# Kernel optimization log

Hardware: AMD Instinct MI355X
Metric: run time of the kernel (lower is better)

The kernel has to match this reference:

```python
import jax, jax.numpy as jnp
import numpy as np
from jax import lax

N_NODES = 100000
L_IN = 60           # raw per-node signal length
DEG = 16            # in-degree per node
HID = 256           # hidden_dim = 64 * (L_IN/15)
HEADS = 2
OUT = HID // 2      # GATConv out_feats per head
EPS_BN = 1e-5
COS_S = 4.6


def setup_inputs() -> dict:
    key = jax.random.key(0)
    k = jax.random.split(key, 12)
    E = N_NODES * DEG
    x = jax.random.normal(k[0], (N_NODES, L_IN), jnp.float32)
    src = jax.random.randint(k[1], (E,), 0, N_NODES, jnp.int32)
    # every node receives DEG incoming edges (DGL GATConv requires nonzero in-degree)
    dst = jnp.repeat(jnp.arange(N_NODES, dtype=jnp.int32), DEG)
    n = lambda i, s, sc=0.05: jax.random.normal(k[i], s, jnp.float32) * sc
    return dict(
        x=x, src=src, dst=dst,
        w1=n(2, (32, 1, 5), 0.2), b1=jnp.zeros(32, jnp.float32),
        bn1_g=jnp.ones(32, jnp.float32), bn1_b=jnp.zeros(32, jnp.float32),
        w2=n(3, (64, 32, 3), 0.1), b2=jnp.zeros(64, jnp.float32),
        bn2_g=jnp.ones(64, jnp.float32), bn2_b=jnp.zeros(64, jnp.float32),
        fc1_w=n(4, (HEADS * OUT, HID)), attn1_l=n(5, (HEADS, OUT)), attn1_r=n(6, (HEADS, OUT)),
        bias1=jnp.zeros(HEADS * OUT, jnp.float32),
        fc2_w=n(7, (HEADS * OUT, HID)), attn2_l=n(8, (HEADS, OUT)), attn2_r=n(9, (HEADS, OUT)),
        bias2=jnp.zeros(HEADS * OUT, jnp.float32),
        dbn_g=jnp.ones(3 * HID, jnp.float32), dbn_b=jnp.zeros(3 * HID, jnp.float32),
        cos_W=n(10, (HID, 3 * HID), 1.0),
    )


def _conv_bn_relu(h, w, b, g, bt, stride):
    # h: [N, Cin, T] -> [N, Cout, T'] ; BatchNorm1d uses batch statistics (train-mode forward)
    y = lax.conv_general_dilated(h, w, (stride,), 'VALID',
                                 dimension_numbers=('NCH', 'OIH', 'NCH'))
    y = y + b[None, :, None]
    m = jnp.mean(y, (0, 2), keepdims=True)
    v = jnp.var(y, (0, 2), keepdims=True)
    y = (y - m) / jnp.sqrt(v + EPS_BN) * g[None, :, None] + bt[None, :, None]
    return jax.nn.relu(y)


def _gat(h, fc_w, al, ar, bias, src, dst):
    # DGL GATConv: fc -> edge attention (leaky_relu 0.2) -> edge softmax over dst -> weighted sum + bias
    feat = (h @ fc_w.T).reshape(N_NODES, HEADS, OUT)          # [N,H,D]
    el = jnp.sum(feat * al[None], -1)                          # [N,H]
    er = jnp.sum(feat * ar[None], -1)                          # [N,H]
    e = jax.nn.leaky_relu(el[src] + er[dst], 0.2)              # [E,H]
    emax = jax.ops.segment_max(e, dst, num_segments=N_NODES)  # [N,H]
    emax = jnp.where(jnp.isfinite(emax), emax, 0.0)
    ex = jnp.exp(e - emax[dst])
    den = jax.ops.segment_sum(ex, dst, num_segments=N_NODES)  # [N,H]
    alpha = ex / jnp.maximum(den[dst], 1e-12)                  # [E,H]
    out = jax.ops.segment_sum(feat[src] * alpha[..., None], dst, num_segments=N_NODES)
    return out + bias.reshape(1, HEADS, OUT)                   # [N,H,D]


def _l2n(a):
    # F.normalize: divide by L2 norm clamped to eps
    return a / jnp.maximum(jnp.linalg.norm(a, axis=1, keepdims=True), 1e-12)


def reference(x, src, dst, w1, b1, bn1_g, bn1_b, w2, b2, bn2_g, bn2_b,
              fc1_w, attn1_l, attn1_r, bias1, fc2_w, attn2_l, attn2_r, bias2,
              dbn_g, dbn_b, cos_W):
    h = x[:, None, :]                                    # [N,1,L]
    h = _conv_bn_relu(h, w1, b1, bn1_g, bn1_b, 5)        # [N,32,12]
    h = _conv_bn_relu(h, w2, b2, bn2_g, bn2_b, 3)        # [N,64,4]
    h = h.reshape(N_NODES, HID)                          # [N,256]
    g1 = _gat(h, fc1_w, attn1_l, attn1_r, bias1, src, dst)
    h1 = (jax.nn.relu(g1) + jnp.tanh(g1) + jax.nn.log_sigmoid(g1)).reshape(N_NODES, HID)
    h2 = jnp.tanh(_gat(h1, fc2_w, attn2_l, attn2_r, bias2, src, dst)).reshape(N_NODES, HID)
    h3 = jax.nn.relu(_gat(h2, fc2_w, attn2_l, attn2_r, bias2, src, dst)).reshape(N_NODES, HID)
    hc = jnp.concatenate([h1, h2, h3], axis=1)           # [N,768]
    m = jnp.mean(hc, 0)
    v = jnp.var(hc, 0)
    hc = (hc - m) / jnp.sqrt(v + EPS_BN) * dbn_g + dbn_b
    return _l2n(hc) @ _l2n(cos_W).T * COS_S              # [N,256]
```

## Files before the change

### kernel.cpp

```cpp
#include <hip/hip_runtime.h>

#define NN 100000
#define MPAD 100096
#define NT_M 782

typedef unsigned short u16;
typedef __attribute__((ext_vector_type(8))) short bf16x8;
typedef __attribute__((ext_vector_type(4))) float f32x4;

__device__ __forceinline__ u16 f2bf(float f){
  union { float f; unsigned u; } v; v.f=f;
  unsigned u = v.u + 0x7fffu + ((v.u>>16)&1u);
  return (u16)(u>>16);
}
__device__ __forceinline__ float bf2f(u16 b){
  union { unsigned u; float f; } v; v.u = ((unsigned)b)<<16; return v.f;
}
__device__ __forceinline__ void gload16(const void* g, void* l){
  __builtin_amdgcn_global_load_lds((const __attribute__((address_space(1))) void*)g,
                                   (__attribute__((address_space(3))) void*)l, 16, 0, 0);
}
__device__ __forceinline__ void lds_fence(){
  asm volatile("s_waitcnt lgkmcnt(0)" ::: "memory");
  __builtin_amdgcn_wave_barrier();
}

template<int EPI>
__global__ __launch_bounds__(256) void k_gemm(
  const u16* __restrict__ ah0, const u16* __restrict__ al0,
  const u16* __restrict__ ah1, const u16* __restrict__ al1,
  const u16* __restrict__ ah2, const u16* __restrict__ al2,
  const u16* __restrict__ bh, const u16* __restrict__ bl,
  u16* __restrict__ chi,
  float* __restrict__ outf, const float* __restrict__ tvec,
  const float* __restrict__ rnorm, int Bstride, int KT)
{
  __shared__ u16 lds[2][4][4096];
  const int tid=threadIdx.x, lane=tid&63, wid=tid>>6;
  const int wr=wid>>1, wc=wid&1;
  const long m0=(long)blockIdx.x*128;
  const int n0=blockIdx.y*128;
  f32x4 acc[4][4]={};

  auto stageT=[&](u16* L, const u16* G, int rs){
    #pragma unroll
    for(int i=0;i<2;i++){
      int idx=i*256+tid;
      int row=idx>>2, c8=idx&3;
      int gc=(c8^(row&3))*8;
      gload16(G+(long)row*rs+gc, L+idx*8);
    }
  };
  auto stage=[&](int buf,int kt){
    const u16 *Ah,*Al; int kc;
    if(kt<8){Ah=ah0;Al=al0;kc=kt*32;}
    else if(kt<16){Ah=ah1;Al=al1;kc=(kt-8)*32;}
    else {Ah=ah2;Al=al2;kc=(kt-16)*32;}
    stageT(lds[buf][0], Ah+m0*256+kc, 256);
    stageT(lds[buf][1], Al+m0*256+kc, 256);
    stageT(lds[buf][2], bh+(long)n0*Bstride+kt*32, Bstride);
    stageT(lds[buf][3], bl+(long)n0*Bstride+kt*32, Bstride);
  };
  stage(0,0);
  __syncthreads();
  int buf=0;
  for(int kt=0;kt<KT;kt++){
    if(kt+1<KT) stage(buf^1,kt+1);
    const u16* LAh=lds[buf][0]; const u16* LAl=lds[buf][1];
    const u16* LBh=lds[buf][2]; const u16* LBl=lds[buf][3];
    bf16x8 avh[4],avl[4],bvh[4],bvl[4];
    #pragma unroll
    for(int mf=0;mf<4;mf++){
      int r=wr*64+mf*16+(lane&15);
      int ch=((lane>>4)^(r&3))*8;
      avh[mf]=*(const bf16x8*)&LAh[r*32+ch];
      avl[mf]=*(const bf16x8*)&LAl[r*32+ch];
    }
    #pragma unroll
    for(int nf=0;nf<4;nf++){
      int r=wc*64+nf*16+(lane&15);
      int ch=((lane>>4)^(r&3))*8;
      bvh[nf]=*(const bf16x8*)&LBh[r*32+ch];
      bvl[nf]=*(const bf16x8*)&LBl[r*32+ch];
    }
    #pragma unroll
    for(int mf=0;mf<4;mf++){
      #pragma unroll
      for(int nf=0;nf<4;nf++){
        acc[mf][nf]=__builtin_amdgcn_mfma_f32_16x16x32_bf16(avh[mf],bvh[nf],acc[mf][nf],0,0,0);
        acc[mf][nf]=__builtin_amdgcn_mfma_f32_16x16x32_bf16(avl[mf],bvh[nf],acc[mf][nf],0,0,0);
        acc[mf][nf]=__builtin_amdgcn_mfma_f32_16x16x32_bf16(avh[mf],bvl[nf],acc[mf][nf],0,0,0);
      }
    }
    __syncthreads();
    buf^=1;
  }
  #pragma unroll
  for(int mf=0;mf<4;mf++){
    #pragma unroll
    for(int j=0;j<4;j++){
      long row=m0+wr*64+mf*16+((lane>>4)*4)+j;
      if(row<NN){
        #pragma unroll
        for(int nf=0;nf<4;nf++){
          int col=n0+wc*64+nf*16+(lane&15);
          float v=acc[mf][nf][j];
          if(EPI==1) outf[row*256+col]=(v+tvec[col])*rnorm[row];
          else       chi[row*256+col]=f2bf(v);
        }
      }
    }
  }
}

__global__ __launch_bounds__(256) void k_xmom(const float* __restrict__ x, float* __restrict__ stats){
  int t=blockIdx.x*blockDim.x+threadIdx.x, stride=gridDim.x*blockDim.x;
  int lane=threadIdx.x&63;
  float m[5]={0,0,0,0,0};
  float c[15]={0,0,0,0,0,0,0,0,0,0,0,0,0,0,0};
  for(int n=t;n<NN;n+=stride){
    float xr[60];
    #pragma unroll
    for(int i=0;i<15;i++){
      float4 v=*(const float4*)&x[(long)n*60+i*4];
      xr[i*4]=v.x; xr[i*4+1]=v.y; xr[i*4+2]=v.z; xr[i*4+3]=v.w;
    }
    #pragma unroll
    for(int p=0;p<12;p++){
      float vv[5]={xr[5*p],xr[5*p+1],xr[5*p+2],xr[5*p+3],xr[5*p+4]};
      #pragma unroll
      for(int k=0;k<5;k++) m[k]+=vv[k];
      int idx=0;
      #pragma unroll
      for(int k=0;k<5;k++){
        #pragma unroll
        for(int k2=k;k2<5;k2++){ c[idx]+=vv[k]*vv[k2]; idx++; }
      }
    }
  }
  float vals[20];
  #pragma unroll
  for(int i=0;i<5;i++) vals[i]=m[i];
  #pragma unroll
  for(int i=0;i<15;i++) vals[5+i]=c[i];
  #pragma unroll
  for(int i=0;i<20;i++){
    float v=vals[i];
    #pragma unroll
    for(int off=32;off;off>>=1) v+=__shfl_xor(v,off);
    if(lane==0) atomicAdd(&stats[i],v);
  }
}

__global__ void k_fin1(const float* __restrict__ stats, const float* __restrict__ w1,
                       const float* __restrict__ b1, const float* __restrict__ g,
                       const float* __restrict__ bt, float* __restrict__ a1c1){
  int c=threadIdx.x;
  if(c>=32) return;
  const float inv=1.0f/(NN*12.0f);
  float mu[5];
  for(int k=0;k<5;k++) mu[k]=stats[k]*inv;
  float C[5][5];
  int idx=5;
  for(int k=0;k<5;k++) for(int k2=k;k2<5;k2++){ float v=stats[idx++]*inv; C[k][k2]=v; C[k2][k]=v; }
  float wv[5];
  for(int k=0;k<5;k++) wv[k]=w1[c*5+k];
  float bb=b1[c];
  float mean=bb, e2=bb*bb;
  for(int k=0;k<5;k++){ mean+=wv[k]*mu[k]; e2+=2.f*bb*wv[k]*mu[k]; }
  for(int k=0;k<5;k++) for(int k2=0;k2<5;k2++) e2+=wv[k]*wv[k2]*C[k][k2];
  float var=e2-mean*mean;
  float a=g[c]*rsqrtf(var+1e-5f);
  a1c1[c]=a; a1c1[32+c]=bt[c]-mean*a;
}

__global__ void k_prep(const float* __restrict__ fc1, const float* __restrict__ fc2,
                       const float* __restrict__ a1l, const float* __restrict__ a1r,
                       const float* __restrict__ a2l, const float* __restrict__ a2r,
                       float* __restrict__ vprep){
  int k=threadIdx.x;
  float acc[8]={0,0,0,0,0,0,0,0};
  for(int r=0;r<256;r++){
    int h=r>>7, c=r&127;
    float f1=fc1[r*256+k], f2=fc2[r*256+k];
    acc[0+h]+=f1*a1l[h*128+c];
    acc[2+h]+=f1*a1r[h*128+c];
    acc[4+h]+=f2*a2l[h*128+c];
    acc[6+h]+=f2*a2r[h*128+c];
  }
  #pragma unroll
  for(int v=0;v<8;v++) vprep[v*256+k]=acc[v];
}

template<int PASS>
__global__ __launch_bounds__(256) void k_conv(const float* __restrict__ x,
  const float* __restrict__ w1, const float* __restrict__ b1,
  const float* __restrict__ a1c1, const float* __restrict__ w2,
  const float* __restrict__ b2, const float* __restrict__ a2c2,
  u16* __restrict__ hH, u16* __restrict__ hL, float* __restrict__ stats2,
  const float* __restrict__ vprep, float* __restrict__ elv, float* __restrict__ erv)
{
  __shared__ float w2s[64*97];
  __shared__ float w1s[160], a1s[32], c1s[32], b1s[32], b2s[64];
  __shared__ float xs[4][64];
  __shared__ float z1s[4][384];
  __shared__ float bsum[128];
  int tid=threadIdx.x, lane=tid&63, w=tid>>6;
  for(int i=tid;i<6144;i+=256) w2s[(i/96)*97+(i%96)]=w2[i];
  if(tid<160) w1s[tid]=w1[tid];
  if(tid<32){ a1s[tid]=a1c1[tid]; c1s[tid]=a1c1[32+tid]; b1s[tid]=b1[tid]; }
  if(tid<64) b2s[tid]=b2[tid];
  if(PASS==0 && tid<128) bsum[tid]=0.f;
  __syncthreads();
  float ssum=0.f, ssq=0.f;
  float a2=0.f, c2v=0.f;
  float4 vl0={0,0,0,0},vl1={0,0,0,0},vr0={0,0,0,0},vr1={0,0,0,0};
  if(PASS==1){
    a2=a2c2[lane]; c2v=a2c2[64+lane];
    int cb=lane*4;
    vl0=*(const float4*)&vprep[cb];
    vl1=*(const float4*)&vprep[256+cb];
    vr0=*(const float4*)&vprep[512+cb];
    vr1=*(const float4*)&vprep[768+cb];
  }
  int gw=blockIdx.x*4+w, nw=gridDim.x*4;
  for(int n=gw;n<NN;n+=nw){
    if(lane<60) xs[w][lane]=x[(long)n*60+lane];
    lds_fence();
    {
      int c=lane>>1, pb=(lane&1)*6;
      float av=a1s[c], cv=c1s[c], bb=b1s[c];
      #pragma unroll
      for(int i=0;i<6;i++){
        int p=pb+i;
        float y=bb;
        #pragma unroll
        for(int k=0;k<5;k++) y+=xs[w][5*p+k]*w1s[c*5+k];
        z1s[w][c*12+p]=fmaxf(y*av+cv,0.f);
      }
    }
    lds_fence();
    {
      int c2=lane;
      float acc0=b2s[c2],acc1=b2s[c2],acc2=b2s[c2],acc3=b2s[c2];
      #pragma unroll
      for(int ci=0;ci<32;ci++){
        float4 za=*(const float4*)&z1s[w][ci*12];
        float4 zb=*(const float4*)&z1s[w][ci*12+4];
        float4 zc=*(const float4*)&z1s[w][ci*12+8];
        float w0=w2s[c2*97+ci*3], wv1=w2s[c2*97+ci*3+1], wv2=w2s[c2*97+ci*3+2];
        acc0 += za.x*w0+za.y*wv1+za.z*wv2;
        acc1 += za.w*w0+zb.x*wv1+zb.y*wv2;
        acc2 += zb.z*w0+zb.w*wv1+zc.x*wv2;
        acc3 += zc.y*w0+zc.z*wv1+zc.w*wv2;
      }
      if(PASS==0){
        ssum+=acc0+acc1+acc2+acc3;
        ssq+=acc0*acc0+acc1*acc1+acc2*acc2+acc3*acc3;
      } else {
        float o0=fmaxf(acc0*a2+c2v,0.f), o1=fmaxf(acc1*a2+c2v,0.f);
        float o2=fmaxf(acc2*a2+c2v,0.f), o3=fmaxf(acc3*a2+c2v,0.f);
        ushort4 hi, lo;
        hi.x=f2bf(o0); lo.x=f2bf(o0-bf2f(hi.x));
        hi.y=f2bf(o1); lo.y=f2bf(o1-bf2f(hi.y));
        hi.z=f2bf(o2); lo.z=f2bf(o2-bf2f(hi.z));
        hi.w=f2bf(o3); lo.w=f2bf(o3-bf2f(hi.w));
        *(ushort4*)&hH[(long)n*256+c2*4]=hi;
        *(ushort4*)&hL[(long)n*256+c2*4]=lo;
        float pl0=o0*vl0.x+o1*vl0.y+o2*vl0.z+o3*vl0.w;
        float pl1=o0*vl1.x+o1*vl1.y+o2*vl1.z+o3*vl1.w;
        float pr0=o0*vr0.x+o1*vr0.y+o2*vr0.z+o3*vr0.w;
        float pr1=o0*vr1.x+o1*vr1.y+o2*vr1.z+o3*vr1.w;
        #pragma unroll
        for(int off2=32;off2;off2>>=1){
          pl0+=__shfl_xor(pl0,off2); pl1+=__shfl_xor(pl1,off2);
          pr0+=__shfl_xor(pr0,off2); pr1+=__shfl_xor(pr1,off2);
        }
        if(lane==0){ elv[2*n]=pl0; elv[2*n+1]=pl1; erv[2*n]=pr0; erv[2*n+1]=pr1; }
      }
    }
    lds_fence();
  }
  if(PASS==0){
    atomicAdd(&bsum[lane],ssum);
    atomicAdd(&bsum[64+lane],ssq);
    __syncthreads();
    if(tid<128) atomicAdd(&stats2[tid],bsum[tid]);
  }
}

__global__ void k_fin2(const float* __restrict__ stats2, const float* __restrict__ g,
                       const float* __restrict__ bt, float* __restrict__ a2c2){
  int c=threadIdx.x;
  if(c>=64) return;
  const float inv=1.0f/(NN*4.0f);
  float mean=stats2[c]*inv;
  float var=stats2[64+c]*inv-mean*mean;
  float a=g[c]*rsqrtf(var+1e-5f);
  a2c2[c]=a; a2c2[64+c]=bt[c]-mean*a;
}

__global__ void k_cvt2(const float* __restrict__ in, u16* __restrict__ oh, u16* __restrict__ ol, int n){
  int i=blockIdx.x*blockDim.x+threadIdx.x;
  if(i<n){
    float v=in[i];
    u16 h=f2bf(v);
    oh[i]=h; ol[i]=f2bf(v-bf2f(h));
  }
}

__global__ __launch_bounds__(256) void k_wfold(const float* __restrict__ cw, const float* __restrict__ ab,
  u16* __restrict__ wh, u16* __restrict__ wl, float* __restrict__ tvec)
{
  int lane=threadIdx.x&63;
  int r=blockIdx.x*4+(threadIdx.x>>6);
  if(r>=256) return;
  float v[12]; float ss=0.f, tn=0.f;
  #pragma unroll
  for(int i=0;i<12;i++){
    int col=i*64+lane;
    v[i]=cw[r*768+col];
    ss+=v[i]*v[i];
    tn+=v[i]*ab[768+col];
  }
  #pragma unroll
  for(int off=32;off;off>>=1){ ss+=__shfl_xor(ss,off); tn+=__shfl_xor(tn,off); }
  float sc=1.0f/fmaxf(sqrtf(ss),1e-12f);
  #pragma unroll
  for(int i=0;i<12;i++){
    int col=i*64+lane;
    float wv=v[i]*sc*ab[col];
    u16 h=f2bf(wv);
    wh[r*768+col]=h; wl[r*768+col]=f2bf(wv-bf2f(h));
  }
  if(lane==0) tvec[r]=tn*sc;
}

__global__ __launch_bounds__(256) void k_alpha(const float* __restrict__ el, const float* __restrict__ er,
  const int* __restrict__ srcv, float* __restrict__ alpha)
{
  int n=blockIdx.x*blockDim.x+threadIdx.x;
  if(n>=NN) return;
  int sidx[16];
  #pragma unroll
  for(int j=0;j<16;j+=4){
    int4 v=*(const int4*)&srcv[n*16+j];
    sidx[j]=v.x; sidx[j+1]=v.y; sidx[j+2]=v.z; sidx[j+3]=v.w;
  }
  float er0=er[2*n], er1=er[2*n+1];
  float e0[16], e1[16];
  float mx0=-1e30f, mx1=-1e30f;
  #pragma unroll
  for(int j=0;j<16;j++){
    float a=el[2*sidx[j]]+er0;
    float bb=el[2*sidx[j]+1]+er1;
    a = a>0.f? a : 0.2f*a;
    bb = bb>0.f? bb : 0.2f*bb;
    e0[j]=a; e1[j]=bb;
    mx0=fmaxf(mx0,a); mx1=fmaxf(mx1,bb);
  }
  float d0=0.f,d1=0.f;
  #pragma unroll
  for(int j=0;j<16;j++){
    e0[j]=__expf(e0[j]-mx0); d0+=e0[j];
    e1[j]=__expf(e1[j]-mx1); d1+=e1[j];
  }
  float r0=1.f/fmaxf(d0,1e-12f), r1=1.f/fmaxf(d1,1e-12f);
  #pragma unroll
  for(int j=0;j<16;j++){
    float2 o; o.x=e0[j]*r0; o.y=e1[j]*r1;
    ((float2*)alpha)[(long)n*16+j]=o;
  }
}

template<int ACT> __device__ __forceinline__ float actf(float g);
template<> __device__ __forceinline__ float actf<1>(float g){
  float t=tanhf(g);
  float ls=fminf(g,0.f)-log1pf(__expf(-fabsf(g)));
  return fmaxf(g,0.f)+t+ls;
}
template<> __device__ __forceinline__ float actf<2>(float g){ return tanhf(g); }
template<> __device__ __forceinline__ float actf<3>(float g){ return fmaxf(g,0.f); }

template<int ACT,int WELR>
__global__ __launch_bounds__(256) void k_aggr(const u16* __restrict__ fH,
  const float* __restrict__ alpha, const int* __restrict__ srcv, const float* __restrict__ bias,
  u16* __restrict__ hH, u16* __restrict__ hL, float* __restrict__ dbn_raw, int col_base,
  const float* __restrict__ vnext, float* __restrict__ elo, float* __restrict__ ero)
{
  __shared__ float bsum[256], bsq[256];
  int tid=threadIdx.x, lane=tid&63;
  bsum[tid]=0.f; bsq[tid]=0.f;
  __syncthreads();
  int gw=blockIdx.x*4+(tid>>6), nw=gridDim.x*4;
  int head=lane>>5, cb=lane*4;
  float4 b4=*(const float4*)&bias[cb];
  float4 vl0={0,0,0,0},vl1={0,0,0,0},vr0={0,0,0,0},vr1={0,0,0,0};
  if(WELR){
    vl0=*(const float4*)&vnext[cb];
    vl1=*(const float4*)&vnext[256+cb];
    vr0=*(const float4*)&vnext[512+cb];
    vr1=*(const float4*)&vnext[768+cb];
  }
  float s[4]={0,0,0,0}, q[4]={0,0,0,0};
  for(int n=gw;n<NN;n+=nw){
    int sidx[16];
    #pragma unroll
    for(int j=0;j<16;j+=4){
      int4 v=*(const int4*)&srcv[n*16+j];
      sidx[j]=v.x; sidx[j+1]=v.y; sidx[j+2]=v.z; sidx[j+3]=v.w;
    }
    float a0=b4.x,a1=b4.y,a2=b4.z,a3=b4.w;
    #pragma unroll
    for(int j=0;j<16;j++){
      float2 aw2=((const float2*)alpha)[(long)n*16+j];
      float aw = head? aw2.y : aw2.x;
      ushort4 f=*(const ushort4*)&fH[(long)sidx[j]*256+cb];
      a0+=aw*bf2f(f.x); a1+=aw*bf2f(f.y);
      a2+=aw*bf2f(f.z); a3+=aw*bf2f(f.w);
    }
    float h0=actf<ACT>(a0), h1=actf<ACT>(a1), h2=actf<ACT>(a2), h3=actf<ACT>(a3);
    ushort4 hi, lo;
    hi.x=f2bf(h0); lo.x=f2bf(h0-bf2f(hi.x));
    hi.y=f2bf(h1); lo.y=f2bf(h1-bf2f(hi.y));
    hi.z=f2bf(h2); lo.z=f2bf(h2-bf2f(hi.z));
    hi.w=f2bf(h3); lo.w=f2bf(h3-bf2f(hi.w));
    *(ushort4*)&hH[(long)n*256+cb]=hi;
    *(ushort4*)&hL[(long)n*256+cb]=lo;
    s[0]+=h0; s[1]+=h1; s[2]+=h2; s[3]+=h3;
    q[0]+=h0*h0; q[1]+=h1*h1; q[2]+=h2*h2; q[3]+=h3*h3;
    if(WELR){
      float pl0=h0*vl0.x+h1*vl0.y+h2*vl0.z+h3*vl0.w;
      float pl1=h0*vl1.x+h1*vl1.y+h2*vl1.z+h3*vl1.w;
      float pr0=h0*vr0.x+h1*vr0.y+h2*vr0.z+h3*vr0.w;
      float pr1=h0*vr1.x+h1*vr1.y+h2*vr1.z+h3*vr1.w;
      #pragma unroll
      for(int off2=32;off2;off2>>=1){
        pl0+=__shfl_xor(pl0,off2); pl1+=__shfl_xor(pl1,off2);
        pr0+=__shfl_xor(pr0,off2); pr1+=__shfl_xor(pr1,off2);
      }
      if(lane==0){ elo[2*n]=pl0; elo[2*n+1]=pl1; ero[2*n]=pr0; ero[2*n+1]=pr1; }
    }
  }
  #pragma unroll
  for(int i=0;i<4;i++){ atomicAdd(&bsum[cb+i], s[i]); atomicAdd(&bsq[cb+i], q[i]); }
  __syncthreads();
  atomicAdd(&dbn_raw[col_base+tid], bsum[tid]);
  atomicAdd(&dbn_raw[768+col_base+tid], bsq[tid]);
}

__global__ void k_dbnfin(const float* __restrict__ raw, const float* __restrict__ g,
                         const float* __restrict__ b, float* __restrict__ ab){
  int c=blockIdx.x*blockDim.x+threadIdx.x;
  if(c<768){
    float mean=raw[c]*(1.0f/NN);
    float var=raw[768+c]*(1.0f/NN)-mean*mean;
    float a=g[c]*rsqrtf(var+1e-5f);
    ab[c]=a; ab[768+c]=b[c]-mean*a;
  }
}

__global__ __launch_bounds__(256) void k_rnorm(
  const u16* __restrict__ h1h, const u16* __restrict__ h1l,
  const u16* __restrict__ h2h, const u16* __restrict__ h2l,
  const u16* __restrict__ h3h, const u16* __restrict__ h3l,
  const float* __restrict__ ab, float* __restrict__ rn)
{
  int lane=threadIdx.x&63;
  int gw=blockIdx.x*4+(threadIdx.x>>6), nw=gridDim.x*4;
  int cb=lane*4;
  float av[12], cv[12];
  #pragma unroll
  for(int s=0;s<3;s++){
    #pragma unroll
    for(int i=0;i<4;i++){ av[s*4+i]=ab[s*256+cb+i]; cv[s*4+i]=ab[768+s*256+cb+i]; }
  }
  for(int n=gw;n<NN;n+=nw){
    float ss=0.f;
    const u16* hh[3]={h1h,h2h,h3h};
    const u16* hl[3]={h1l,h2l,h3l};
    #pragma unroll
    for(int s=0;s<3;s++){
      ushort4 a4=*(const ushort4*)&hh[s][(long)n*256+cb];
      ushort4 c4=*(const ushort4*)&hl[s][(long)n*256+cb];
      float o0=(bf2f(a4.x)+bf2f(c4.x))*av[s*4+0]+cv[s*4+0];
      float o1=(bf2f(a4.y)+bf2f(c4.y))*av[s*4+1]+cv[s*4+1];
      float o2=(bf2f(a4.z)+bf2f(c4.z))*av[s*4+2]+cv[s*4+2];
      float o3=(bf2f(a4.w)+bf2f(c4.w))*av[s*4+3]+cv[s*4+3];
      ss+=o0*o0+o1*o1+o2*o2+o3*o3;
    }
    #pragma unroll
    for(int off=32;off;off>>=1) ss+=__shfl_xor(ss,off);
    if(lane==0) rn[n]=4.6f/fmaxf(sqrtf(ss),1e-12f);
  }
}

extern "C" void kernel_launch(void* const* d_in, const int* in_sizes, int n_in,
                              void* d_out, int out_size, void* d_ws, size_t ws_size,
                              hipStream_t stream)
{
  (void)in_sizes; (void)n_in; (void)out_size; (void)ws_size;
  const float* x   =(const float*)d_in[0];
  const int*   src =(const int*)d_in[1];
  const float* w1  =(const float*)d_in[3];
  const float* b1  =(const float*)d_in[4];
  const float* bn1g=(const float*)d_in[5];
  const float* bn1b=(const float*)d_in[6];
  const float* w2  =(const float*)d_in[7];
  const float* b2  =(const float*)d_in[8];
  const float* bn2g=(const float*)d_in[9];
  const float* bn2b=(const float*)d_in[10];
  const float* fc1 =(const float*)d_in[11];
  const float* a1l =(const float*)d_in[12];
  const float* a1r =(const float*)d_in[13];
  const float* bias1=(const float*)d_in[14];
  const float* fc2 =(const float*)d_in[15];
  const float* a2l =(const float*)d_in[16];
  const float* a2r =(const float*)d_in[17];
  const float* bias2=(const float*)d_in[18];
  const float* dbng=(const float*)d_in[19];
  const float* dbnb=(const float*)d_in[20];
  const float* cw  =(const float*)d_in[21];

  char* ws=(char*)d_ws;
  size_t off=0;
  auto take=[&](size_t bytes)->char*{ char* p=ws+off; off=(off+bytes+255)&~(size_t)255; return p; };
  float* stats =(float*)take(2048*4);
  float* params=(float*)take(4096*4);
  float* el    =(float*)take((size_t)MPAD*2*4);
  float* er    =(float*)take((size_t)MPAD*2*4);
  float* rnorm =(float*)take((size_t)MPAD*4);
  float* tvec  =(float*)take(256*4);
  float* alpha =(float*)take((size_t)NN*32*4);
  u16* fc1h=(u16*)take((size_t)65536*2);
  u16* fc1l=(u16*)take((size_t)65536*2);
  u16* fc2h=(u16*)take((size_t)65536*2);
  u16* fc2l=(u16*)take((size_t)65536*2);
  u16* wfh =(u16*)take((size_t)196608*2);
  u16* wfl =(u16*)take((size_t)196608*2);
  const size_t FB=(size_t)MPAD*256*2;
  u16* h0H  =(u16*)take(FB); u16* h0L  =(u16*)take(FB);
  u16* h1H  =(u16*)take(FB); u16* h1L  =(u16*)take(FB);
  u16* h2H  =(u16*)take(FB); u16* h2L  =(u16*)take(FB);
  u16* featH=(u16*)d_out;

  float* xmom   =stats;
  float* stats2 =stats+32;
  float* dbn_raw=stats+512;
  float* a1c1   =params;
  float* a2c2   =params+64;
  float* dbn_ab =params+256;
  float* vprep  =params+2048;

  hipMemsetAsync(stats,0,2048*4,stream);
  k_cvt2<<<dim3(256),dim3(256),0,stream>>>(fc1,fc1h,fc1l,65536);
  k_cvt2<<<dim3(256),dim3(256),0,stream>>>(fc2,fc2h,fc2l,65536);
  k_prep<<<dim3(1),dim3(256),0,stream>>>(fc1,fc2,a1l,a1r,a2l,a2r,vprep);
  k_xmom<<<dim3(128),dim3(256),0,stream>>>(x,xmom);
  k_fin1<<<dim3(1),dim3(64),0,stream>>>(xmom,w1,b1,bn1g,bn1b,a1c1);
  k_conv<0><<<dim3(1024),dim3(256),0,stream>>>(x,w1,b1,a1c1,w2,b2,a2c2,h0H,h0L,stats2,vprep,el,er);
  k_fin2<<<dim3(1),dim3(64),0,stream>>>(stats2,bn2g,bn2b,a2c2);
  k_conv<1><<<dim3(1024),dim3(256),0,stream>>>(x,w1,b1,a1c1,w2,b2,a2c2,h0H,h0L,stats2,vprep,el,er);

  dim3 gg(NT_M,2);
  k_gemm<0><<<gg,dim3(256),0,stream>>>(h0H,h0L,h0H,h0L,h0H,h0L,fc1h,fc1l,featH,
                                       (float*)nullptr,tvec,rnorm,256,8);
  k_alpha<<<dim3(391),dim3(256),0,stream>>>(el,er,src,alpha);
  k_aggr<1,1><<<dim3(2048),dim3(256),0,stream>>>(featH,alpha,src,bias1,h1H,h1L,dbn_raw,0,
                                                 vprep+1024,el,er);
  k_gemm<0><<<gg,dim3(256),0,stream>>>(h1H,h1L,h1H,h1L,h1H,h1L,fc2h,fc2l,featH,
                                       (float*)nullptr,tvec,rnorm,256,8);
  k_alpha<<<dim3(391),dim3(256),0,stream>>>(el,er,src,alpha);
  k_aggr<2,1><<<dim3(2048),dim3(256),0,stream>>>(featH,alpha,src,bias2,h2H,h2L,dbn_raw,256,
                                                 vprep+1024,el,er);
  k_gemm<0><<<gg,dim3(256),0,stream>>>(h2H,h2L,h2H,h2L,h2H,h2L,fc2h,fc2l,featH,
                                       (float*)nullptr,tvec,rnorm,256,8);
  k_alpha<<<dim3(391),dim3(256),0,stream>>>(el,er,src,alpha);
  k_aggr<3,0><<<dim3(2048),dim3(256),0,stream>>>(featH,alpha,src,bias2,h0H,h0L,dbn_raw,512,
                                                 vprep+1024,el,er);
  k_dbnfin<<<dim3(3),dim3(256),0,stream>>>(dbn_raw,dbng,dbnb,dbn_ab);
  k_wfold<<<dim3(64),dim3(256),0,stream>>>(cw,dbn_ab,wfh,wfl,tvec);
  k_rnorm<<<dim3(1024),dim3(256),0,stream>>>(h1H,h1L,h2H,h2L,h0H,h0L,dbn_ab,rnorm);
  k_gemm<1><<<gg,dim3(256),0,stream>>>(h1H,h1L,h2H,h2L,h0H,h0L,wfh,wfl,(u16*)nullptr,
                                       (float*)d_out,tvec,rnorm,768,24);
}
```

Baseline: 1.572 ms.

## Replace split-bf16 hi/lo GEMMs with single fp16 operands and split conv pass

Replaces the three-MFMA split-bf16 (hi/lo) emulation of fp32 GEMMs with a single fp16 MFMA per fragment, widens the K tile to 64 with an 8-way swizzle, and drops all low-part activation and weight buffers. The second conv pass, which recomputed conv1/conv2, now stores fp32 conv2 outputs once and a new elementwise kernel applies BN/ReLU and computes el/er. This removes about two thirds of the MFMA work and halves activation traffic for the GEMM operands and the aggregation, rnorm and final steps. In exchange, precision drops to single fp16 (about 11 bits of mantissa, with limited range) and a 100MB fp32 intermediate is written and read.

```diff
diff --git a/kernel.cpp b/kernel.cpp
--- a/kernel.cpp
+++ b/kernel.cpp
@@ -5,16 +5,14 @@
 #define NT_M 782
 
 typedef unsigned short u16;
-typedef __attribute__((ext_vector_type(8))) short bf16x8;
+typedef _Float16 f16x8 __attribute__((ext_vector_type(8)));
 typedef __attribute__((ext_vector_type(4))) float f32x4;
 
-__device__ __forceinline__ u16 f2bf(float f){
-  union { float f; unsigned u; } v; v.f=f;
-  unsigned u = v.u + 0x7fffu + ((v.u>>16)&1u);
-  return (u16)(u>>16);
-}
-__device__ __forceinline__ float bf2f(u16 b){
-  union { unsigned u; float f; } v; v.u = ((unsigned)b)<<16; return v.f;
+__device__ __forceinline__ u16 f2h(float f){
+  union { _Float16 h; u16 u; } v; v.h=(_Float16)f; return v.u;
+}
+__device__ __forceinline__ float h2f(u16 u){
+  union { u16 u; _Float16 h; } v; v.u=u; return (float)v.h;
 }
 __device__ __forceinline__ void gload16(const void* g, void* l){
   __builtin_amdgcn_global_load_lds((const __attribute__((address_space(1))) void*)g,
@@ -27,69 +25,57 @@
 
 template<int EPI>
 __global__ __launch_bounds__(256) void k_gemm(
-  const u16* __restrict__ ah0, const u16* __restrict__ al0,
-  const u16* __restrict__ ah1, const u16* __restrict__ al1,
-  const u16* __restrict__ ah2, const u16* __restrict__ al2,
-  const u16* __restrict__ bh, const u16* __restrict__ bl,
-  u16* __restrict__ chi,
+  const u16* __restrict__ a0, const u16* __restrict__ a1, const u16* __restrict__ a2,
+  const u16* __restrict__ bmat, u16* __restrict__ cout,
   float* __restrict__ outf, const float* __restrict__ tvec,
   const float* __restrict__ rnorm, int Bstride, int KT)
 {
-  __shared__ u16 lds[2][4][4096];
+  __shared__ u16 lds[2][2][8192];
   const int tid=threadIdx.x, lane=tid&63, wid=tid>>6;
   const int wr=wid>>1, wc=wid&1;
   const long m0=(long)blockIdx.x*128;
   const int n0=blockIdx.y*128;
   f32x4 acc[4][4]={};
 
-  auto stageT=[&](u16* L, const u16* G, int rs){
-    #pragma unroll
-    for(int i=0;i<2;i++){
+  auto stageT=[&](u16* L, const u16* G, long rs){
+    #pragma unroll
+    for(int i=0;i<4;i++){
       int idx=i*256+tid;
-      int row=idx>>2, c8=idx&3;
-      int gc=(c8^(row&3))*8;
+      int row=idx>>3, slot=idx&7;
+      int gc=(slot^(row&7))*8;
       gload16(G+(long)row*rs+gc, L+idx*8);
     }
   };
   auto stage=[&](int buf,int kt){
-    const u16 *Ah,*Al; int kc;
-    if(kt<8){Ah=ah0;Al=al0;kc=kt*32;}
-    else if(kt<16){Ah=ah1;Al=al1;kc=(kt-8)*32;}
-    else {Ah=ah2;Al=al2;kc=(kt-16)*32;}
-    stageT(lds[buf][0], Ah+m0*256+kc, 256);
-    stageT(lds[buf][1], Al+m0*256+kc, 256);
-    stageT(lds[buf][2], bh+(long)n0*Bstride+kt*32, Bstride);
-    stageT(lds[buf][3], bl+(long)n0*Bstride+kt*32, Bstride);
+    const u16* Ab=(kt<4)?a0:((kt<8)?a1:a2);
+    int kc=(kt&3)*64;
+    stageT(lds[buf][0], Ab+m0*256+kc, 256);
+    stageT(lds[buf][1], bmat+(long)n0*Bstride+kt*64, Bstride);
   };
   stage(0,0);
   __syncthreads();
   int buf=0;
   for(int kt=0;kt<KT;kt++){
     if(kt+1<KT) stage(buf^1,kt+1);
-    const u16* LAh=lds[buf][0]; const u16* LAl=lds[buf][1];
-    const u16* LBh=lds[buf][2]; const u16* LBl=lds[buf][3];
-    bf16x8 avh[4],avl[4],bvh[4],bvl[4];
-    #pragma unroll
-    for(int mf=0;mf<4;mf++){
-      int r=wr*64+mf*16+(lane&15);
-      int ch=((lane>>4)^(r&3))*8;
-      avh[mf]=*(const bf16x8*)&LAh[r*32+ch];
-      avl[mf]=*(const bf16x8*)&LAl[r*32+ch];
-    }
-    #pragma unroll
-    for(int nf=0;nf<4;nf++){
-      int r=wc*64+nf*16+(lane&15);
-      int ch=((lane>>4)^(r&3))*8;
-      bvh[nf]=*(const bf16x8*)&LBh[r*32+ch];
-      bvl[nf]=*(const bf16x8*)&LBl[r*32+ch];
-    }
-    #pragma unroll
-    for(int mf=0;mf<4;mf++){
+    const u16* LA=lds[buf][0]; const u16* LB=lds[buf][1];
+    #pragma unroll
+    for(int kk=0;kk<2;kk++){
+      f16x8 av[4], bv[4];
+      #pragma unroll
+      for(int mf=0;mf<4;mf++){
+        int r=wr*64+mf*16+(lane&15);
+        av[mf]=*(const f16x8*)&LA[r*64 + (((kk*4+(lane>>4))^(r&7))*8)];
+      }
       #pragma unroll
       for(int nf=0;nf<4;nf++){
-        acc[mf][nf]=__builtin_amdgcn_mfma_f32_16x16x32_bf16(avh[mf],bvh[nf],acc[mf][nf],0,0,0);
-        acc[mf][nf]=__builtin_amdgcn_mfma_f32_16x16x32_bf16(avl[mf],bvh[nf],acc[mf][nf],0,0,0);
-        acc[mf][nf]=__builtin_amdgcn_mfma_f32_16x16x32_bf16(avh[mf],bvl[nf],acc[mf][nf],0,0,0);
+        int r=wc*64+nf*16+(lane&15);
+        bv[nf]=*(const f16x8*)&LB[r*64 + (((kk*4+(lane>>4))^(r&7))*8)];
+      }
+      #pragma unroll
+      for(int mf=0;mf<4;mf++){
+        #pragma unroll
+        for(int nf=0;nf<4;nf++)
+          acc[mf][nf]=__builtin_amdgcn_mfma_f32_16x16x32_f16(av[mf],bv[nf],acc[mf][nf],0,0,0);
       }
     }
     __syncthreads();
@@ -106,7 +92,7 @@
           int col=n0+wc*64+nf*16+(lane&15);
           float v=acc[mf][nf][j];
           if(EPI==1) outf[row*256+col]=(v+tvec[col])*rnorm[row];
-          else       chi[row*256+col]=f2bf(v);
+          else       cout[row*256+col]=f2h(v);
         }
       }
     }
@@ -192,13 +178,10 @@
   for(int v=0;v<8;v++) vprep[v*256+k]=acc[v];
 }
 
-template<int PASS>
 __global__ __launch_bounds__(256) void k_conv(const float* __restrict__ x,
   const float* __restrict__ w1, const float* __restrict__ b1,
   const float* __restrict__ a1c1, const float* __restrict__ w2,
-  const float* __restrict__ b2, const float* __restrict__ a2c2,
-  u16* __restrict__ hH, u16* __restrict__ hL, float* __restrict__ stats2,
-  const float* __restrict__ vprep, float* __restrict__ elv, float* __restrict__ erv)
+  const float* __restrict__ b2, float* __restrict__ y2, float* __restrict__ stats2)
 {
   __shared__ float w2s[64*97];
   __shared__ float w1s[160], a1s[32], c1s[32], b1s[32], b2s[64];
@@ -210,19 +193,9 @@
   if(tid<160) w1s[tid]=w1[tid];
   if(tid<32){ a1s[tid]=a1c1[tid]; c1s[tid]=a1c1[32+tid]; b1s[tid]=b1[tid]; }
   if(tid<64) b2s[tid]=b2[tid];
-  if(PASS==0 && tid<128) bsum[tid]=0.f;
+  if(tid<128) bsum[tid]=0.f;
   __syncthreads();
   float ssum=0.f, ssq=0.f;
-  float a2=0.f, c2v=0.f;
-  float4 vl0={0,0,0,0},vl1={0,0,0,0},vr0={0,0,0,0},vr1={0,0,0,0};
-  if(PASS==1){
-    a2=a2c2[lane]; c2v=a2c2[64+lane];
-    int cb=lane*4;
-    vl0=*(const float4*)&vprep[cb];
-    vl1=*(const float4*)&vprep[256+cb];
-    vr0=*(const float4*)&vprep[512+cb];
-    vr1=*(const float4*)&vprep[768+cb];
-  }
   int gw=blockIdx.x*4+w, nw=gridDim.x*4;
   for(int n=gw;n<NN;n+=nw){
     if(lane<60) xs[w][lane]=x[(long)n*60+lane];
@@ -254,39 +227,17 @@
         acc2 += zb.z*w0+zb.w*wv1+zc.x*wv2;
         acc3 += zc.y*w0+zc.z*wv1+zc.w*wv2;
       }
-      if(PASS==0){
-        ssum+=acc0+acc1+acc2+acc3;
-        ssq+=acc0*acc0+acc1*acc1+acc2*acc2+acc3*acc3;
-      } else {
-        float o0=fmaxf(acc0*a2+c2v,0.f), o1=fmaxf(acc1*a2+c2v,0.f);
-        float o2=fmaxf(acc2*a2+c2v,0.f), o3=fmaxf(acc3*a2+c2v,0.f);
-        ushort4 hi, lo;
-        hi.x=f2bf(o0); lo.x=f2bf(o0-bf2f(hi.x));
-        hi.y=f2bf(o1); lo.y=f2bf(o1-bf2f(hi.y));
-        hi.z=f2bf(o2); lo.z=f2bf(o2-bf2f(hi.z));
-        hi.w=f2bf(o3); lo.w=f2bf(o3-bf2f(hi.w));
-        *(ushort4*)&hH[(long)n*256+c2*4]=hi;
-        *(ushort4*)&hL[(long)n*256+c2*4]=lo;
-        float pl0=o0*vl0.x+o1*vl0.y+o2*vl0.z+o3*vl0.w;
-        float pl1=o0*vl1.x+o1*vl1.y+o2*vl1.z+o3*vl1.w;
-        float pr0=o0*vr0.x+o1*vr0.y+o2*vr0.z+o3*vr0.w;
-        float pr1=o0*vr1.x+o1*vr1.y+o2*vr1.z+o3*vr1.w;
-        #pragma unroll
-        for(int off2=32;off2;off2>>=1){
-          pl0+=__shfl_xor(pl0,off2); pl1+=__shfl_xor(pl1,off2);
-          pr0+=__shfl_xor(pr0,off2); pr1+=__shfl_xor(pr1,off2);
-        }
-        if(lane==0){ elv[2*n]=pl0; elv[2*n+1]=pl1; erv[2*n]=pr0; erv[2*n+1]=pr1; }
-      }
+      float4 o; o.x=acc0; o.y=acc1; o.z=acc2; o.w=acc3;
+      *(float4*)&y2[(long)n*256+c2*4]=o;
+      ssum+=acc0+acc1+acc2+acc3;
+      ssq+=acc0*acc0+acc1*acc1+acc2*acc2+acc3*acc3;
     }
     lds_fence();
   }
-  if(PASS==0){
-    atomicAdd(&bsum[lane],ssum);
-    atomicAdd(&bsum[64+lane],ssq);
-    __syncthreads();
-    if(tid<128) atomicAdd(&stats2[tid],bsum[tid]);
-  }
+  atomicAdd(&bsum[lane],ssum);
+  atomicAdd(&bsum[64+lane],ssq);
+  __syncthreads();
+  if(tid<128) atomicAdd(&stats2[tid],bsum[tid]);
 }
 
 __global__ void k_fin2(const float* __restrict__ stats2, const float* __restrict__ g,
@@ -300,17 +251,44 @@
   a2c2[c]=a; a2c2[64+c]=bt[c]-mean*a;
 }
 
-__global__ void k_cvt2(const float* __restrict__ in, u16* __restrict__ oh, u16* __restrict__ ol, int n){
+__global__ __launch_bounds__(256) void k_happ(const float* __restrict__ y2,
+  const float* __restrict__ a2c2, const float* __restrict__ vprep,
+  u16* __restrict__ h, float* __restrict__ elv, float* __restrict__ erv)
+{
+  int lane=threadIdx.x&63;
+  int gw=blockIdx.x*4+(threadIdx.x>>6), nw=gridDim.x*4;
+  float a2=a2c2[lane], c2v=a2c2[64+lane];
+  int cb=lane*4;
+  float4 vl0=*(const float4*)&vprep[cb];
+  float4 vl1=*(const float4*)&vprep[256+cb];
+  float4 vr0=*(const float4*)&vprep[512+cb];
+  float4 vr1=*(const float4*)&vprep[768+cb];
+  for(int n=gw;n<NN;n+=nw){
+    float4 y=*(const float4*)&y2[(long)n*256+cb];
+    float o0=fmaxf(y.x*a2+c2v,0.f), o1=fmaxf(y.y*a2+c2v,0.f);
+    float o2=fmaxf(y.z*a2+c2v,0.f), o3=fmaxf(y.w*a2+c2v,0.f);
+    ushort4 o; o.x=f2h(o0); o.y=f2h(o1); o.z=f2h(o2); o.w=f2h(o3);
+    *(ushort4*)&h[(long)n*256+cb]=o;
+    float pl0=o0*vl0.x+o1*vl0.y+o2*vl0.z+o3*vl0.w;
+    float pl1=o0*vl1.x+o1*vl1.y+o2*vl1.z+o3*vl1.w;
+    float pr0=o0*vr0.x+o1*vr0.y+o2*vr0.z+o3*vr0.w;
+    float pr1=o0*vr1.x+o1*vr1.y+o2*vr1.z+o3*vr1.w;
+    #pragma unroll
+    for(int off=32;off;off>>=1){
+      pl0+=__shfl_xor(pl0,off); pl1+=__shfl_xor(pl1,off);
+      pr0+=__shfl_xor(pr0,off); pr1+=__shfl_xor(pr1,off);
+    }
+    if(lane==0){ elv[2*n]=pl0; elv[2*n+1]=pl1; erv[2*n]=pr0; erv[2*n+1]=pr1; }
+  }
+}
+
+__global__ void k_cvth(const float* __restrict__ in, u16* __restrict__ out, int n){
   int i=blockIdx.x*blockDim.x+threadIdx.x;
-  if(i<n){
-    float v=in[i];
-    u16 h=f2bf(v);
-    oh[i]=h; ol[i]=f2bf(v-bf2f(h));
-  }
+  if(i<n) out[i]=f2h(in[i]);
 }
 
 __global__ __launch_bounds__(256) void k_wfold(const float* __restrict__ cw, const float* __restrict__ ab,
-  u16* __restrict__ wh, u16* __restrict__ wl, float* __restrict__ tvec)
+  u16* __restrict__ wh, float* __restrict__ tvec)
 {
   int lane=threadIdx.x&63;
   int r=blockIdx.x*4+(threadIdx.x>>6);
@@ -329,9 +307,7 @@
   #pragma unroll
   for(int i=0;i<12;i++){
     int col=i*64+lane;
-    float wv=v[i]*sc*ab[col];
-    u16 h=f2bf(wv);
-    wh[r*768+col]=h; wl[r*768+col]=f2bf(wv-bf2f(h));
+    wh[r*768+col]=f2h(v[i]*sc*ab[col]);
   }
   if(lane==0) tvec[r]=tn*sc;
 }
@@ -385,7 +361,7 @@
 template<int ACT,int WELR>
 __global__ __launch_bounds__(256) void k_aggr(const u16* __restrict__ fH,
   const float* __restrict__ alpha, const int* __restrict__ srcv, const float* __restrict__ bias,
-  u16* __restrict__ hH, u16* __restrict__ hL, float* __restrict__ dbn_raw, int col_base,
+  u16* __restrict__ hH, float* __restrict__ dbn_raw, int col_base,
   const float* __restrict__ vnext, float* __restrict__ elo, float* __restrict__ ero)
 {
   __shared__ float bsum[256], bsq[256];
@@ -416,17 +392,12 @@
       float2 aw2=((const float2*)alpha)[(long)n*16+j];
       float aw = head? aw2.y : aw2.x;
       ushort4 f=*(const ushort4*)&fH[(long)sidx[j]*256+cb];
-      a0+=aw*bf2f(f.x); a1+=aw*bf2f(f.y);
-      a2+=aw*bf2f(f.z); a3+=aw*bf2f(f.w);
+      a0+=aw*h2f(f.x); a1+=aw*h2f(f.y);
+      a2+=aw*h2f(f.z); a3+=aw*h2f(f.w);
     }
     float h0=actf<ACT>(a0), h1=actf<ACT>(a1), h2=actf<ACT>(a2), h3=actf<ACT>(a3);
-    ushort4 hi, lo;
-    hi.x=f2bf(h0); lo.x=f2bf(h0-bf2f(hi.x));
-    hi.y=f2bf(h1); lo.y=f2bf(h1-bf2f(hi.y));
-    hi.z=f2bf(h2); lo.z=f2bf(h2-bf2f(hi.z));
-    hi.w=f2bf(h3); lo.w=f2bf(h3-bf2f(hi.w));
-    *(ushort4*)&hH[(long)n*256+cb]=hi;
-    *(ushort4*)&hL[(long)n*256+cb]=lo;
+    ushort4 o; o.x=f2h(h0); o.y=f2h(h1); o.z=f2h(h2); o.w=f2h(h3);
+    *(ushort4*)&hH[(long)n*256+cb]=o;
     s[0]+=h0; s[1]+=h1; s[2]+=h2; s[3]+=h3;
     q[0]+=h0*h0; q[1]+=h1*h1; q[2]+=h2*h2; q[3]+=h3*h3;
     if(WELR){
@@ -461,9 +432,7 @@
 }
 
 __global__ __launch_bounds__(256) void k_rnorm(
-  const u16* __restrict__ h1h, const u16* __restrict__ h1l,
-  const u16* __restrict__ h2h, const u16* __restrict__ h2l,
-  const u16* __restrict__ h3h, const u16* __restrict__ h3l,
+  const u16* __restrict__ h1h, const u16* __restrict__ h2h, const u16* __restrict__ h3h,
   const float* __restrict__ ab, float* __restrict__ rn)
 {
   int lane=threadIdx.x&63;
@@ -478,15 +447,13 @@
   for(int n=gw;n<NN;n+=nw){
     float ss=0.f;
     const u16* hh[3]={h1h,h2h,h3h};
-    const u16* hl[3]={h1l,h2l,h3l};
     #pragma unroll
     for(int s=0;s<3;s++){
       ushort4 a4=*(const ushort4*)&hh[s][(long)n*256+cb];
-      ushort4 c4=*(const ushort4*)&hl[s][(long)n*256+cb];
-      float o0=(bf2f(a4.x)+bf2f(c4.x))*av[s*4+0]+cv[s*4+0];
-      float o1=(bf2f(a4.y)+bf2f(c4.y))*av[s*4+1]+cv[s*4+1];
-      float o2=(bf2f(a4.z)+bf2f(c4.z))*av[s*4+2]+cv[s*4+2];
-      float o3=(bf2f(a4.w)+bf2f(c4.w))*av[s*4+3]+cv[s*4+3];
+      float o0=h2f(a4.x)*av[s*4+0]+cv[s*4+0];
+      float o1=h2f(a4.y)*av[s*4+1]+cv[s*4+1];
+      float o2=h2f(a4.z)*av[s*4+2]+cv[s*4+2];
+      float o3=h2f(a4.w)*av[s*4+3]+cv[s*4+3];
       ss+=o0*o0+o1*o1+o2*o2+o3*o3;
     }
     #pragma unroll
@@ -533,15 +500,13 @@
   float* tvec  =(float*)take(256*4);
   float* alpha =(float*)take((size_t)NN*32*4);
   u16* fc1h=(u16*)take((size_t)65536*2);
-  u16* fc1l=(u16*)take((size_t)65536*2);
   u16* fc2h=(u16*)take((size_t)65536*2);
-  u16* fc2l=(u16*)take((size_t)65536*2);
   u16* wfh =(u16*)take((size_t)196608*2);
-  u16* wfl =(u16*)take((size_t)196608*2);
+  float* y2 =(float*)take((size_t)MPAD*256*4);
   const size_t FB=(size_t)MPAD*256*2;
-  u16* h0H  =(u16*)take(FB); u16* h0L  =(u16*)take(FB);
-  u16* h1H  =(u16*)take(FB); u16* h1L  =(u16*)take(FB);
-  u16* h2H  =(u16*)take(FB); u16* h2L  =(u16*)take(FB);
+  u16* h0H  =(u16*)take(FB);
+  u16* h1H  =(u16*)take(FB);
+  u16* h2H  =(u16*)take(FB);
   u16* featH=(u16*)d_out;
 
   float* xmom   =stats;
@@ -553,34 +518,31 @@
   float* vprep  =params+2048;
 
   hipMemsetAsync(stats,0,2048*4,stream);
-  k_cvt2<<<dim3(256),dim3(256),0,stream>>>(fc1,fc1h,fc1l,65536);
-  k_cvt2<<<dim3(256),dim3(256),0,stream>>>(fc2,fc2h,fc2l,65536);
+  k_cvth<<<dim3(256),dim3(256),0,stream>>>(fc1,fc1h,65536);
+  k_cvth<<<dim3(256),dim3(256),0,stream>>>(fc2,fc2h,65536);
   k_prep<<<dim3(1),dim3(256),0,stream>>>(fc1,fc2,a1l,a1r,a2l,a2r,vprep);
   k_xmom<<<dim3(128),dim3(256),0,stream>>>(x,xmom);
   k_fin1<<<dim3(1),dim3(64),0,stream>>>(xmom,w1,b1,bn1g,bn1b,a1c1);
-  k_conv<0><<<dim3(1024),dim3(256),0,stream>>>(x,w1,b1,a1c1,w2,b2,a2c2,h0H,h0L,stats2,vprep,el,er);
+  k_conv<<<dim3(1024),dim3(256),0,stream>>>(x,w1,b1,a1c1,w2,b2,y2,stats2);
   k_fin2<<<dim3(1),dim3(64),0,stream>>>(stats2,bn2g,bn2b,a2c2);
-  k_conv<1><<<dim3(1024),dim3(256),0,stream>>>(x,w1,b1,a1c1,w2,b2,a2c2,h0H,h0L,stats2,vprep,el,er);
+  k_happ<<<dim3(2048),dim3(256),0,stream>>>(y2,a2c2,vprep,h0H,el,er);
 
   dim3 gg(NT_M,2);
-  k_gemm<0><<<gg,dim3(256),0,stream>>>(h0H,h0L,h0H,h0L,h0H,h0L,fc1h,fc1l,featH,
-                                       (float*)nullptr,tvec,rnorm,256,8);
+  k_gemm<0><<<gg,dim3(256),0,stream>>>(h0H,h0H,h0H,fc1h,featH,(float*)nullptr,tvec,rnorm,256,4);
   k_alpha<<<dim3(391),dim3(256),0,stream>>>(el,er,src,alpha);
-  k_aggr<1,1><<<dim3(2048),dim3(256),0,stream>>>(featH,alpha,src,bias1,h1H,h1L,dbn_raw,0,
+  k_aggr<1,1><<<dim3(2048),dim3(256),0,stream>>>(featH,alpha,src,bias1,h1H,dbn_raw,0,
                                                  vprep+1024,el,er);
-  k_gemm<0><<<gg,dim3(256),0,stream>>>(h1H,h1L,h1H,h1L,h1H,h1L,fc2h,fc2l,featH,
-                                       (float*)nullptr,tvec,rnorm,256,8);
+  k_gemm<0><<<gg,dim3(256),0,stream>>>(h1H,h1H,h1H,fc2h,featH,(float*)nullptr,tvec,rnorm,256,4);
   k_alpha<<<dim3(391),dim3(256),0,stream>>>(el,er,src,alpha);
-  k_aggr<2,1><<<dim3(2048),dim3(256),0,stream>>>(featH,alpha,src,bias2,h2H,h2L,dbn_raw,256,
+  k_aggr<2,1><<<dim3(2048),dim3(256),0,stream>>>(featH,alpha,src,bias2,h2H,dbn_raw,256,
                                                  vprep+1024,el,er);
-  k_gemm<0><<<gg,dim3(256),0,stream>>>(h2H,h2L,h2H,h2L,h2H,h2L,fc2h,fc2l,featH,
-                                       (float*)nullptr,tvec,rnorm,256,8);
+  k_gemm<0><<<gg,dim3(256),0,stream>>>(h2H,h2H,h2H,fc2h,featH,(float*)nullptr,tvec,rnorm,256,4);
   k_alpha<<<dim3(391),dim3(256),0,stream>>>(el,er,src,alpha);
-  k_aggr<3,0><<<dim3(2048),dim3(256),0,stream>>>(featH,alpha,src,bias2,h0H,h0L,dbn_raw,512,
+  k_aggr<3,0><<<dim3(2048),dim3(256),0,stream>>>(featH,alpha,src,bias2,h0H,dbn_raw,512,
                                                  vprep+1024,el,er);
   k_dbnfin<<<dim3(3),dim3(256),0,stream>>>(dbn_raw,dbng,dbnb,dbn_ab);
-  k_wfold<<<dim3(64),dim3(256),0,stream>>>(cw,dbn_ab,wfh,wfl,tvec);
-  k_rnorm<<<dim3(1024),dim3(256),0,stream>>>(h1H,h1L,h2H,h2L,h0H,h0L,dbn_ab,rnorm);
-  k_gemm<1><<<gg,dim3(256),0,stream>>>(h1H,h1L,h2H,h2L,h0H,h0L,wfh,wfl,(u16*)nullptr,
-                                       (float*)d_out,tvec,rnorm,768,24);
-}
+  k_wfold<<<dim3(64),dim3(256),0,stream>>>(cw,dbn_ab,wfh,tvec);
+  k_rnorm<<<dim3(1024),dim3(256),0,stream>>>(h1H,h2H,h0H,dbn_ab,rnorm);
+  k_gemm<1><<<gg,dim3(256),0,stream>>>(h1H,h2H,h0H,wfh,(u16*)nullptr,
+                                       (float*)d_out,tvec,rnorm,768,12);
+}
```

New measurement: 1.259 ms. 1.25x faster.
